# Performance work log

Measured on AMD Instinct MI355X. Metric: run time of the kernel, lower is better.

The kernel has to match this reference:

```python
import jax, jax.numpy as jnp
import numpy as np

INPUT_DIM = 128
OUTPUT_DIM = 64
EMBED_DIM = 3
B, S = 16, 2048
EPS = 1e-6


def setup_inputs() -> dict:
    key = jax.random.key(0)
    ks = jax.random.split(key, 8)
    scale = 0.05
    return {
        "x": jax.random.normal(ks[0], (B, S, INPUT_DIM), dtype=jnp.float32),
        "threshold": jnp.asarray(0.1, dtype=jnp.float32),
        "w1": jax.random.normal(ks[1], (INPUT_DIM, 2 * EMBED_DIM), dtype=jnp.float32) * scale,
        "b1": jnp.zeros((2 * EMBED_DIM,), dtype=jnp.float32),
        "w2": jax.random.normal(ks[2], (2 * EMBED_DIM, EMBED_DIM), dtype=jnp.float32) * scale,
        "b2": jnp.zeros((EMBED_DIM,), dtype=jnp.float32),
        "w3": jax.random.normal(ks[3], (4, OUTPUT_DIM), dtype=jnp.float32) * scale,
        "b3": jnp.zeros((OUTPUT_DIM,), dtype=jnp.float32),
    }


def reference(x, threshold, w1, b1, w2, b2, w3, b3):
    # phase-space embedding: Linear -> ReLU -> Linear   [B,S,E]
    h = jnp.maximum(x @ w1 + b1, 0.0) @ w2 + b2
    Bsz, Slen, _ = h.shape

    # pairwise euclidean distances (torch.cdist) per batch element [B,S,S]
    sq = jnp.sum(h * h, axis=-1)                         # [B,S]
    d2 = sq[:, :, None] + sq[:, None, :] - 2.0 * jnp.einsum('bse,bte->bst', h, h)
    dist = jnp.sqrt(jnp.maximum(d2, 0.0))

    # per-sample threshold = sigmoid(theta) * max(dist)
    thr = jax.nn.sigmoid(threshold) * jnp.max(dist, axis=(1, 2), keepdims=True)
    R = (dist < thr).astype(h.dtype)                     # recurrence matrix [B,S,S]

    total = jnp.sum(R, axis=(1, 2))                      # [B]
    rr = total / (Slen * Slen)                           # recurrence rate

    # sum of super-diagonals with offsets 1..min(S,10)-1
    idx = jnp.arange(Slen)
    off = idx[None, :] - idx[:, None]
    dmask = ((off >= 1) & (off <= min(Slen, 10) - 1)).astype(h.dtype)  # [S,S]
    diag_structures = jnp.einsum('bst,st->b', R, dmask)
    det = diag_structures / (total + EPS)

    # vertical structures: per column (over rows, axis=1), count runs of length >= 2.
    # a run of length>=2 starts at row i iff R[i]=1, R[i-1]=0 (or i=0), R[i+1]=1.
    prev = jnp.pad(R[:, :-1, :], ((0, 0), (1, 0), (0, 0)))
    nxt = jnp.pad(R[:, 1:, :], ((0, 0), (0, 1), (0, 0)))
    vert_structures = jnp.sum(R * (1.0 - prev) * nxt, axis=(1, 2))
    lam = vert_structures / (total + EPS)

    # 'entropy' term as written in the original (R is 0/1 valued)
    entr = -jnp.sum(R * jnp.log(R + EPS), axis=(1, 2))

    metrics = jnp.stack([rr, det, lam, entr], axis=-1)   # [B,4]
    return jnp.maximum(metrics @ w3 + b3, 0.0)           # [B,output_dim]
```

## Files before the change

### kernel.cpp

```cpp
#include <hip/hip_runtime.h>
#include <math.h>

#define B_ 16
#define S_ 2048
#define IN_DIM 128
#define E2 6
#define E_ 3
#define OUT_DIM 64


__global__ __launch_bounds__(256) void embed_kernel(
    const float* __restrict__ x, const float* __restrict__ w1,
    const float* __restrict__ b1, const float* __restrict__ w2,
    const float* __restrict__ b2, float* __restrict__ hws)
{
    int wave = threadIdx.x >> 6;
    int lane = threadIdx.x & 63;
    int rig  = lane >> 4;
    int g    = lane & 15;
    int row  = blockIdx.x * 16 + wave * 4 + rig;

    const float4* x4 = (const float4*)(x + (size_t)row * IN_DIM) + g * 2;
    float4 xa = x4[0];
    float4 xb = x4[1];
    float xk[8] = {xa.x, xa.y, xa.z, xa.w, xb.x, xb.y, xb.z, xb.w};

    const float4* w14 = (const float4*)(w1 + g * 8 * E2);
    float w[48];
#pragma unroll
    for (int t = 0; t < 12; ++t) ((float4*)w)[t] = w14[t];

    float a[E2];
#pragma unroll
    for (int q = 0; q < E2; ++q) a[q] = 0.f;
#pragma unroll
    for (int kk = 0; kk < 8; ++kk) {
#pragma unroll
        for (int q = 0; q < E2; ++q)
            a[q] = fmaf(xk[kk], w[kk * E2 + q], a[q]);
    }

#pragma unroll
    for (int q = 0; q < E2; ++q) {
#pragma unroll
        for (int off = 8; off >= 1; off >>= 1)
            a[q] += __shfl_xor(a[q], off, 64);
    }

    if (g == 0) {
        float r[E2];
#pragma unroll
        for (int q = 0; q < E2; ++q) r[q] = fmaxf(a[q] + b1[q], 0.f);
        float h[E_];
#pragma unroll
        for (int e = 0; e < E_; ++e) {
            float s = b2[e];
#pragma unroll
            for (int q = 0; q < E2; ++q) s += r[q] * w2[q * E_ + e];
            h[e] = s;
        }
        float sq = h[0] * h[0] + h[1] * h[1] + h[2] * h[2];
        ((float4*)hws)[row] = make_float4(h[0], h[1], h[2], sq);
    }
}

__global__ __launch_bounds__(256) void max_kernel(
    const float4* __restrict__ h4, float* __restrict__ pmax, int* __restrict__ fincnt)
{
    if (blockIdx.x == 0 && threadIdx.x == 0) *fincnt = 0;
    int bid = blockIdx.x;
    int b  = bid >> 5;
    int rb = bid & 31;
    int r0 = rb * 64;
    const float4* hb = h4 + (size_t)b * S_;
    __shared__ float4 sh[64];
    if (threadIdx.x < 64) {
        float4 rv = hb[r0 + threadIdx.x];
        sh[threadIdx.x] = make_float4(-2.f * rv.x, -2.f * rv.y, -2.f * rv.z, rv.w);
    }
    float4 hj[5];
#pragma unroll
    for (int c = 0; c < 5; ++c) {
        int j = (r0 + c * 256 + threadIdx.x) & (S_ - 1);
        hj[c] = hb[j];
    }
    __syncthreads();
    float mc[5];
#pragma unroll
    for (int c = 0; c < 5; ++c) mc[c] = -1e30f;
    float4 rv = sh[63];
#pragma unroll 4
    for (int k = 62; k >= 0; --k) {
        float4 nx = sh[k];
#pragma unroll
        for (int c = 0; c < 5; ++c) {
            float t = fmaf(hj[c].x, rv.x,
                      fmaf(hj[c].y, rv.y,
                      fmaf(hj[c].z, rv.z, rv.w)));
            mc[c] = fmaxf(mc[c], t);
        }
        rv = nx;
    }
#pragma unroll
    for (int c = 0; c < 5; ++c) {
        float t = fmaf(hj[c].x, rv.x,
                  fmaf(hj[c].y, rv.y,
                  fmaf(hj[c].z, rv.z, rv.w)));
        mc[c] = fmaxf(mc[c], t);
    }
    float m = -1e30f;
#pragma unroll
    for (int c = 0; c < 5; ++c) m = fmaxf(m, mc[c] + hj[c].w);
    m = fmaxf(m, 0.f);
#pragma unroll
    for (int off = 32; off >= 1; off >>= 1)
        m = fmaxf(m, __shfl_xor(m, off, 64));
    __shared__ float wmax[4];
    int lane = threadIdx.x & 63, wave = threadIdx.x >> 6;
    if (lane == 0) wmax[wave] = m;
    __syncthreads();
    if (threadIdx.x == 0) {
        float mm = fmaxf(fmaxf(wmax[0], wmax[1]), fmaxf(wmax[2], wmax[3]));
        pmax[bid] = mm;
    }
}

__global__ __launch_bounds__(256) void stats_kernel(
    const float4* __restrict__ h4, const float* __restrict__ theta,
    const float* __restrict__ pmax, int4* __restrict__ pstat,
    int* __restrict__ fincnt,
    const float* __restrict__ w3, const float* __restrict__ b3,
    float* __restrict__ out)
{
    int bid = blockIdx.x;
    int b  = bid >> 5;
    int rb = bid & 31;
    int r0 = rb * 64;
    const float4* hb = h4 + (size_t)b * S_;
    __shared__ float4 sh[66];
    if (threadIdx.x < 66) {
        int r = r0 - 1 + threadIdx.x;
        r = r < 0 ? 0 : (r >= S_ ? S_ - 1 : r);
        float4 rv = hb[r];
        sh[threadIdx.x] = make_float4(-2.f * rv.x, -2.f * rv.y, -2.f * rv.z, rv.w);
    }
    float4 hj[8];
#pragma unroll
    for (int c = 0; c < 8; ++c) hj[c] = hb[c * 256 + threadIdx.x];
    __syncthreads();

    int lane = threadIdx.x & 63;
    float pm = pmax[b * 32 + (lane & 31)];
#pragma unroll
    for (int off = 16; off >= 1; off >>= 1)
        pm = fmaxf(pm, __shfl_xor(pm, off, 64));
    float maxd2 = pm;

    float sig   = 1.f / (1.f + expf(-theta[0]));
    float thr2  = sig * sig * maxd2;
    float thrc[8];
#pragma unroll
    for (int c = 0; c < 8; ++c) thrc[c] = thr2 - hj[c].w;

    unsigned mlo[8], mhi[8];
#pragma unroll
    for (int c = 0; c < 8; ++c) { mlo[c] = 0u; mhi[c] = 0u; }

    float4 rv = sh[64];
#pragma unroll 4
    for (int k = 63; k >= 32; --k) {
        float4 nx = sh[k];
#pragma unroll
        for (int c = 0; c < 8; ++c) {
            float t = fmaf(hj[c].x, rv.x,
                      fmaf(hj[c].y, rv.y,
                      fmaf(hj[c].z, rv.z, rv.w)));
            mhi[c] = mhi[c] * 2u + ((t < thrc[c]) ? 1u : 0u);
        }
        rv = nx;
    }
#pragma unroll 4
    for (int k = 31; k >= 0; --k) {
        float4 nx = sh[k];
#pragma unroll
        for (int c = 0; c < 8; ++c) {
            float t = fmaf(hj[c].x, rv.x,
                      fmaf(hj[c].y, rv.y,
                      fmaf(hj[c].z, rv.z, rv.w)));
            mlo[c] = mlo[c] * 2u + ((t < thrc[c]) ? 1u : 0u);
        }
        rv = nx;
    }
    float4 pr = rv;
    float4 nxr = sh[65];

    int total = 0, diag = 0, vert = 0;
#pragma unroll
    for (int c = 0; c < 8; ++c) {
        int j = c * 256 + threadIdx.x;
        unsigned long long m = ((unsigned long long)mhi[c] << 32) | mlo[c];
        total += __popcll(m);
        float tp = fmaf(hj[c].x, pr.x, fmaf(hj[c].y, pr.y, fmaf(hj[c].z, pr.z, pr.w)));
        float tn = fmaf(hj[c].x, nxr.x, fmaf(hj[c].y, nxr.y, fmaf(hj[c].z, nxr.z, nxr.w)));
        unsigned long long prevbit = (r0 > 0) ? ((tp < thrc[c]) ? 1ull : 0ull) : 0ull;
        unsigned long long nextbit = (r0 + 64 < S_) ? ((tn < thrc[c]) ? 1ull : 0ull) : 0ull;
        unsigned long long notprev = ~((m << 1) | prevbit);
        vert += __popcll(m & notprev & ((m >> 1) | (nextbit << 63)));
        int lo = j - 9 - r0, hi = j - 1 - r0;
        if (hi >= 0 && lo <= 63) {
            int l = lo < 0 ? 0 : lo;
            int h = hi > 63 ? 63 : hi;
            unsigned long long bandm = ((1ull << (h - l + 1)) - 1ull) << l;
            diag += __popcll(m & bandm);
        }
    }

    int dv = (diag << 16) | vert;
#pragma unroll
    for (int off = 32; off >= 1; off >>= 1) {
        total += __shfl_xor(total, off, 64);
        dv    += __shfl_xor(dv,    off, 64);
    }
    __shared__ int wsum[4][2];
    __shared__ int slast;
    int wave = threadIdx.x >> 6;
    if (lane == 0) { wsum[wave][0] = total; wsum[wave][1] = dv; }
    __syncthreads();
    if (threadIdx.x == 0) {
        int t = 0, d = 0, v = 0;
#pragma unroll
        for (int w = 0; w < 4; ++w) {
            t += wsum[w][0];
            d += wsum[w][1] >> 16;
            v += wsum[w][1] & 0xFFFF;
        }
        pstat[bid] = make_int4(t, d, v, 0);
        __threadfence();
        int done = atomicAdd(fincnt, 1);
        slast = (done == (int)gridDim.x - 1) ? 1 : 0;
    }
    __syncthreads();
    if (slast == 0) return;

    __threadfence();
    __shared__ float stot[16], sdia[16], sver[16];
    int tid = threadIdx.x;
    if (tid < 16) {
        int t = 0, d = 0, v = 0;
        for (int i = 0; i < 32; ++i) {
            int4 p = pstat[tid * 32 + i];
            t += p.x; d += p.y; v += p.z;
        }
        stot[tid] = (float)t; sdia[tid] = (float)d; sver[tid] = (float)v;
    }
    __syncthreads();
#pragma unroll
    for (int q = 0; q < 4; ++q) {
        int idx = q * 256 + tid;
        int bb = idx >> 6, o = idx & 63;
        float tt = stot[bb], dd = sdia[bb], vv = sver[bb];
        float rr  = tt / (float)(S_ * S_);
        float det = dd / (tt + 1e-6f);
        float lam = vv / (tt + 1e-6f);
        float entr = -tt * logf(1.0f + 1e-6f);
        float r = b3[o] + rr  * w3[0 * OUT_DIM + o]
                        + det * w3[1 * OUT_DIM + o]
                        + lam * w3[2 * OUT_DIM + o]
                        + entr * w3[3 * OUT_DIM + o];
        out[idx] = fmaxf(r, 0.f);
    }
}

extern "C" void kernel_launch(void* const* d_in, const int* in_sizes, int n_in,
                              void* d_out, int out_size, void* d_ws, size_t ws_size,
                              hipStream_t stream) {
    const float* x     = (const float*)d_in[0];
    const float* theta = (const float*)d_in[1];
    const float* w1    = (const float*)d_in[2];
    const float* b1    = (const float*)d_in[3];
    const float* w2    = (const float*)d_in[4];
    const float* b2    = (const float*)d_in[5];
    const float* w3    = (const float*)d_in[6];
    const float* b3    = (const float*)d_in[7];
    float* out = (float*)d_out;
    float* hws = (float*)d_ws;
    float* pmax = (float*)((char*)d_ws + 524288);
    int4*  pstat = (int4*)((char*)d_ws + 526336);
    int*   fincnt = (int*)((char*)d_ws + 534528);

    hipLaunchKernelGGL(embed_kernel, dim3(B_ * S_ / 16), dim3(256), 0, stream,
                       x, w1, b1, w2, b2, hws);
    hipLaunchKernelGGL(max_kernel, dim3(B_ * 32), dim3(256), 0, stream,
                       (const float4*)hws, pmax, fincnt);
    hipLaunchKernelGGL(stats_kernel, dim3(B_ * 32), dim3(256), 0, stream,
                       (const float4*)hws, theta, pmax, pstat, fincnt, w3, b3, out);
}
```

Baseline: 107.0 us.

## Fuse embed, max and stats kernels into one kernel with per-batch atomic barriers

Replaces the three separate launches (embedding, max-distance, stats) with a single 512-block kernel. Each block first computes 64 embedding rows, then waits on a per-batch atomic counter barrier before the max pass, and on a second counter before the stats pass. The aim is to remove the launch gaps and kernel-boundary syncs between stages. In exchange, it relies on all blocks being co-resident and adds spin-waiting. Counter reset is guarded by a persistent magic flag that is never cleared, so counters left at 32 by an earlier call may let blocks pass the barrier before the embeddings are written.

```diff
diff --git a/kernel.cpp b/kernel.cpp
--- a/kernel.cpp
+++ b/kernel.cpp
@@ -8,90 +8,127 @@
 #define E_ 3
 #define OUT_DIM 64
 
-
-__global__ __launch_bounds__(256) void embed_kernel(
+#define SCOPE_AGENT __HIP_MEMORY_SCOPE_AGENT
+#define MAGIC 0xA5F00D5EC0FFEE17ull
+
+
+__global__ __launch_bounds__(256, 2) void fused_kernel(
     const float* __restrict__ x, const float* __restrict__ w1,
     const float* __restrict__ b1, const float* __restrict__ w2,
-    const float* __restrict__ b2, float* __restrict__ hws)
+    const float* __restrict__ b2, const float* __restrict__ theta,
+    const float* __restrict__ w3, const float* __restrict__ b3,
+    float* __restrict__ hws, float* __restrict__ pmax,
+    int4* __restrict__ pstat, int* __restrict__ aux,
+    unsigned long long* __restrict__ flag, float* __restrict__ out)
 {
-    int wave = threadIdx.x >> 6;
-    int lane = threadIdx.x & 63;
-    int rig  = lane >> 4;
-    int g    = lane & 15;
-    int row  = blockIdx.x * 16 + wave * 4 + rig;
-
-    const float4* x4 = (const float4*)(x + (size_t)row * IN_DIM) + g * 2;
-    float4 xa = x4[0];
-    float4 xb = x4[1];
-    float xk[8] = {xa.x, xa.y, xa.z, xa.w, xb.x, xb.y, xb.z, xb.w};
-
-    const float4* w14 = (const float4*)(w1 + g * 8 * E2);
-    float w[48];
-#pragma unroll
-    for (int t = 0; t < 12; ++t) ((float4*)w)[t] = w14[t];
-
-    float a[E2];
-#pragma unroll
-    for (int q = 0; q < E2; ++q) a[q] = 0.f;
-#pragma unroll
-    for (int kk = 0; kk < 8; ++kk) {
-#pragma unroll
-        for (int q = 0; q < E2; ++q)
-            a[q] = fmaf(xk[kk], w[kk * E2 + q], a[q]);
-    }
-
-#pragma unroll
-    for (int q = 0; q < E2; ++q) {
-#pragma unroll
-        for (int off = 8; off >= 1; off >>= 1)
-            a[q] += __shfl_xor(a[q], off, 64);
-    }
-
-    if (g == 0) {
-        float r[E2];
-#pragma unroll
-        for (int q = 0; q < E2; ++q) r[q] = fmaxf(a[q] + b1[q], 0.f);
-        float h[E_];
-#pragma unroll
-        for (int e = 0; e < E_; ++e) {
-            float s = b2[e];
-#pragma unroll
-            for (int q = 0; q < E2; ++q) s += r[q] * w2[q * E_ + e];
-            h[e] = s;
-        }
-        float sq = h[0] * h[0] + h[1] * h[1] + h[2] * h[2];
-        ((float4*)hws)[row] = make_float4(h[0], h[1], h[2], sq);
-    }
-}
-
-__global__ __launch_bounds__(256) void max_kernel(
-    const float4* __restrict__ h4, float* __restrict__ pmax, int* __restrict__ fincnt)
-{
-    if (blockIdx.x == 0 && threadIdx.x == 0) *fincnt = 0;
-    int bid = blockIdx.x;
-    int b  = bid >> 5;
-    int rb = bid & 31;
-    int r0 = rb * 64;
-    const float4* hb = h4 + (size_t)b * S_;
-    __shared__ float4 sh[64];
-    if (threadIdx.x < 64) {
-        float4 rv = hb[r0 + threadIdx.x];
-        sh[threadIdx.x] = make_float4(-2.f * rv.x, -2.f * rv.y, -2.f * rv.z, rv.w);
-    }
-    float4 hj[5];
-#pragma unroll
-    for (int c = 0; c < 5; ++c) {
-        int j = (r0 + c * 256 + threadIdx.x) & (S_ - 1);
-        hj[c] = hb[j];
-    }
-    __syncthreads();
-    float mc[5];
-#pragma unroll
-    for (int c = 0; c < 5; ++c) mc[c] = -1e30f;
-    float4 rv = sh[63];
+    int bid = blockIdx.x, tid = threadIdx.x;
+    int wave = tid >> 6, lane = tid & 63;
+    int b = bid >> 5, rb = bid & 31, r0 = rb * 64;
+
+    if (bid == 0 && tid == 0) {
+        for (int i = 0; i < 33; ++i) aux[i] = 0;
+        __threadfence();
+        __hip_atomic_store(flag, MAGIC, __ATOMIC_RELEASE, SCOPE_AGENT);
+    }
+
+    {
+        int rig = lane >> 4;
+        int g   = lane & 15;
+
+        const float4* w14 = (const float4*)(w1 + g * 8 * E2);
+        float w[48];
+#pragma unroll
+        for (int t = 0; t < 12; ++t) ((float4*)w)[t] = w14[t];
+
+        const float* xrow = x + (size_t)(bid * 64 + wave * 4 + rig) * IN_DIM;
+        float4 xs[8];
+#pragma unroll
+        for (int it = 0; it < 4; ++it) {
+            const float4* x4 = (const float4*)(xrow + it * 16 * IN_DIM) + g * 2;
+            xs[2 * it]     = x4[0];
+            xs[2 * it + 1] = x4[1];
+        }
+
+#pragma unroll
+        for (int it = 0; it < 4; ++it) {
+            float xk[8] = {xs[2*it].x, xs[2*it].y, xs[2*it].z, xs[2*it].w,
+                           xs[2*it+1].x, xs[2*it+1].y, xs[2*it+1].z, xs[2*it+1].w};
+            float a[E2];
+#pragma unroll
+            for (int q = 0; q < E2; ++q) a[q] = 0.f;
+#pragma unroll
+            for (int kk = 0; kk < 8; ++kk) {
+#pragma unroll
+                for (int q = 0; q < E2; ++q)
+                    a[q] = fmaf(xk[kk], w[kk * E2 + q], a[q]);
+            }
+#pragma unroll
+            for (int q = 0; q < E2; ++q) {
+#pragma unroll
+                for (int off = 8; off >= 1; off >>= 1)
+                    a[q] += __shfl_xor(a[q], off, 64);
+            }
+            if (g == 0) {
+                float r[E2];
+#pragma unroll
+                for (int q = 0; q < E2; ++q) r[q] = fmaxf(a[q] + b1[q], 0.f);
+                float h[E_];
+#pragma unroll
+                for (int e = 0; e < E_; ++e) {
+                    float s = b2[e];
+#pragma unroll
+                    for (int q = 0; q < E2; ++q) s += r[q] * w2[q * E_ + e];
+                    h[e] = s;
+                }
+                float sq = h[0] * h[0] + h[1] * h[1] + h[2] * h[2];
+                int row = bid * 64 + it * 16 + wave * 4 + rig;
+                ((float4*)hws)[row] = make_float4(h[0], h[1], h[2], sq);
+            }
+        }
+    }
+
+    __syncthreads();
+    if (tid == 0) {
+        while (__hip_atomic_load(flag, __ATOMIC_ACQUIRE, SCOPE_AGENT) != MAGIC)
+            __builtin_amdgcn_s_sleep(8);
+        __threadfence();
+        __hip_atomic_fetch_add(&aux[b], 1, __ATOMIC_RELEASE, SCOPE_AGENT);
+        while (__hip_atomic_load(&aux[b], __ATOMIC_ACQUIRE, SCOPE_AGENT) < 32)
+            __builtin_amdgcn_s_sleep(8);
+    }
+    __syncthreads();
+    __threadfence();
+
+    const float4* hb = (const float4*)hws + (size_t)b * S_;
+    __shared__ float4 sh[66];
+    if (tid < 64) {
+        float4 rv = hb[r0 + tid];
+        sh[tid] = make_float4(-2.f * rv.x, -2.f * rv.y, -2.f * rv.z, rv.w);
+    }
+    {
+        float4 hj[5];
+#pragma unroll
+        for (int c = 0; c < 5; ++c) {
+            int j = (r0 + c * 256 + tid) & (S_ - 1);
+            hj[c] = hb[j];
+        }
+        __syncthreads();
+        float mc[5];
+#pragma unroll
+        for (int c = 0; c < 5; ++c) mc[c] = -1e30f;
+        float4 rv = sh[63];
 #pragma unroll 4
-    for (int k = 62; k >= 0; --k) {
-        float4 nx = sh[k];
+        for (int k = 62; k >= 0; --k) {
+            float4 nx = sh[k];
+#pragma unroll
+            for (int c = 0; c < 5; ++c) {
+                float t = fmaf(hj[c].x, rv.x,
+                          fmaf(hj[c].y, rv.y,
+                          fmaf(hj[c].z, rv.z, rv.w)));
+                mc[c] = fmaxf(mc[c], t);
+            }
+            rv = nx;
+        }
 #pragma unroll
         for (int c = 0; c < 5; ++c) {
             float t = fmaf(hj[c].x, rv.x,
@@ -99,57 +136,42 @@
                       fmaf(hj[c].z, rv.z, rv.w)));
             mc[c] = fmaxf(mc[c], t);
         }
-        rv = nx;
-    }
-#pragma unroll
-    for (int c = 0; c < 5; ++c) {
-        float t = fmaf(hj[c].x, rv.x,
-                  fmaf(hj[c].y, rv.y,
-                  fmaf(hj[c].z, rv.z, rv.w)));
-        mc[c] = fmaxf(mc[c], t);
-    }
-    float m = -1e30f;
-#pragma unroll
-    for (int c = 0; c < 5; ++c) m = fmaxf(m, mc[c] + hj[c].w);
-    m = fmaxf(m, 0.f);
-#pragma unroll
-    for (int off = 32; off >= 1; off >>= 1)
-        m = fmaxf(m, __shfl_xor(m, off, 64));
-    __shared__ float wmax[4];
-    int lane = threadIdx.x & 63, wave = threadIdx.x >> 6;
-    if (lane == 0) wmax[wave] = m;
-    __syncthreads();
-    if (threadIdx.x == 0) {
-        float mm = fmaxf(fmaxf(wmax[0], wmax[1]), fmaxf(wmax[2], wmax[3]));
-        pmax[bid] = mm;
-    }
-}
-
-__global__ __launch_bounds__(256) void stats_kernel(
-    const float4* __restrict__ h4, const float* __restrict__ theta,
-    const float* __restrict__ pmax, int4* __restrict__ pstat,
-    int* __restrict__ fincnt,
-    const float* __restrict__ w3, const float* __restrict__ b3,
-    float* __restrict__ out)
-{
-    int bid = blockIdx.x;
-    int b  = bid >> 5;
-    int rb = bid & 31;
-    int r0 = rb * 64;
-    const float4* hb = h4 + (size_t)b * S_;
-    __shared__ float4 sh[66];
-    if (threadIdx.x < 66) {
-        int r = r0 - 1 + threadIdx.x;
+        float m = -1e30f;
+#pragma unroll
+        for (int c = 0; c < 5; ++c) m = fmaxf(m, mc[c] + hj[c].w);
+        m = fmaxf(m, 0.f);
+#pragma unroll
+        for (int off = 32; off >= 1; off >>= 1)
+            m = fmaxf(m, __shfl_xor(m, off, 64));
+        __shared__ float wmax[4];
+        if (lane == 0) wmax[wave] = m;
+        __syncthreads();
+        if (tid == 0) {
+            float mm = fmaxf(fmaxf(wmax[0], wmax[1]), fmaxf(wmax[2], wmax[3]));
+            pmax[bid] = mm;
+        }
+    }
+
+    if (tid == 0) {
+        __threadfence();
+        __hip_atomic_fetch_add(&aux[16 + b], 1, __ATOMIC_RELEASE, SCOPE_AGENT);
+        while (__hip_atomic_load(&aux[16 + b], __ATOMIC_ACQUIRE, SCOPE_AGENT) < 32)
+            __builtin_amdgcn_s_sleep(8);
+    }
+    __syncthreads();
+    __threadfence();
+
+    if (tid < 66) {
+        int r = r0 - 1 + tid;
         r = r < 0 ? 0 : (r >= S_ ? S_ - 1 : r);
         float4 rv = hb[r];
-        sh[threadIdx.x] = make_float4(-2.f * rv.x, -2.f * rv.y, -2.f * rv.z, rv.w);
+        sh[tid] = make_float4(-2.f * rv.x, -2.f * rv.y, -2.f * rv.z, rv.w);
     }
     float4 hj[8];
 #pragma unroll
-    for (int c = 0; c < 8; ++c) hj[c] = hb[c * 256 + threadIdx.x];
-    __syncthreads();
-
-    int lane = threadIdx.x & 63;
+    for (int c = 0; c < 8; ++c) hj[c] = hb[c * 256 + tid];
+    __syncthreads();
+
     float pm = pmax[b * 32 + (lane & 31)];
 #pragma unroll
     for (int off = 16; off >= 1; off >>= 1)
@@ -197,7 +219,7 @@
     int total = 0, diag = 0, vert = 0;
 #pragma unroll
     for (int c = 0; c < 8; ++c) {
-        int j = c * 256 + threadIdx.x;
+        int j = c * 256 + tid;
         unsigned long long m = ((unsigned long long)mhi[c] << 32) | mlo[c];
         total += __popcll(m);
         float tp = fmaf(hj[c].x, pr.x, fmaf(hj[c].y, pr.y, fmaf(hj[c].z, pr.z, pr.w)));
@@ -223,10 +245,9 @@
     }
     __shared__ int wsum[4][2];
     __shared__ int slast;
-    int wave = threadIdx.x >> 6;
     if (lane == 0) { wsum[wave][0] = total; wsum[wave][1] = dv; }
     __syncthreads();
-    if (threadIdx.x == 0) {
+    if (tid == 0) {
         int t = 0, d = 0, v = 0;
 #pragma unroll
         for (int w = 0; w < 4; ++w) {
@@ -236,7 +257,7 @@
         }
         pstat[bid] = make_int4(t, d, v, 0);
         __threadfence();
-        int done = atomicAdd(fincnt, 1);
+        int done = __hip_atomic_fetch_add(&aux[32], 1, __ATOMIC_ACQ_REL, SCOPE_AGENT);
         slast = (done == (int)gridDim.x - 1) ? 1 : 0;
     }
     __syncthreads();
@@ -244,7 +265,6 @@
 
     __threadfence();
     __shared__ float stot[16], sdia[16], sver[16];
-    int tid = threadIdx.x;
     if (tid < 16) {
         int t = 0, d = 0, v = 0;
         for (int i = 0; i < 32; ++i) {
@@ -286,12 +306,10 @@
     float* hws = (float*)d_ws;
     float* pmax = (float*)((char*)d_ws + 524288);
     int4*  pstat = (int4*)((char*)d_ws + 526336);
-    int*   fincnt = (int*)((char*)d_ws + 534528);
-
-    hipLaunchKernelGGL(embed_kernel, dim3(B_ * S_ / 16), dim3(256), 0, stream,
-                       x, w1, b1, w2, b2, hws);
-    hipLaunchKernelGGL(max_kernel, dim3(B_ * 32), dim3(256), 0, stream,
-                       (const float4*)hws, pmax, fincnt);
-    hipLaunchKernelGGL(stats_kernel, dim3(B_ * 32), dim3(256), 0, stream,
-                       (const float4*)hws, theta, pmax, pstat, fincnt, w3, b3, out);
+    int*   aux = (int*)((char*)d_ws + 534528);
+    unsigned long long* flag = (unsigned long long*)((char*)d_ws + 534664);
+
+    hipLaunchKernelGGL(fused_kernel, dim3(B_ * 32), dim3(256), 0, stream,
+                       x, w1, b1, w2, b2, theta, w3, b3,
+                       hws, pmax, pstat, aux, flag, out);
 }
```

Result: slower. 239.7 us (+124.1%).
